# Performance work log

Hardware: AMD Instinct MI355X
Metric: run time of the kernel (lower is better)

## Reference

```python
import jax, jax.numpy as jnp
import numpy as np

B, T, D, H = 2, 4096, 512, 8
DH = D // H  # dim_head = 64


def setup_inputs() -> dict:
    key = jax.random.key(0)
    ks = jax.random.split(key, 10)
    s = 1.0 / np.sqrt(D)
    x = jax.random.normal(ks[0], (B, T, D), dtype=jnp.float32)
    Wq = jax.random.uniform(ks[1], (D, D), jnp.float32, -s, s)
    Wk = jax.random.uniform(ks[2], (D, D), jnp.float32, -s, s)
    Wv = jax.random.uniform(ks[3], (D, D), jnp.float32, -s, s)
    Wo = jax.random.uniform(ks[4], (D, D), jnp.float32, -s, s)
    bq = jnp.zeros((D,), jnp.float32)
    bk = jnp.zeros((D,), jnp.float32)
    bv = jnp.zeros((D,), jnp.float32)
    bo = jnp.zeros((D,), jnp.float32)
    mask = jax.random.randint(ks[5], (1, 1, T, T), 0, 2).astype(bool)
    return {"x": x, "Wq": Wq, "bq": bq, "Wk": Wk, "bk": bk,
            "Wv": Wv, "bv": bv, "Wo": Wo, "bo": bo, "mask": mask}


def reference(x, Wq, bq, Wk, bk, Wv, bv, Wo, bo, mask):
    # QKV projections (self-attention: Q=K=V=x)
    def split_heads(t):
        return t.reshape(B, T, H, DH).transpose(0, 2, 1, 3)  # (B,H,T,DH)
    Q = split_heads(x @ Wq + bq)
    K = split_heads(x @ Wk + bk)
    V = split_heads(x @ Wv + bv)
    # scaled dot-product attention with additive mask penalty (as in source)
    scores = jnp.einsum('bhqd,bhkd->bhqk', Q, K) / np.sqrt(DH)
    scores = scores + (~mask).astype(scores.dtype) * (-1e9)
    att_w = jax.nn.softmax(scores, axis=-1)
    O = jnp.einsum('bhqk,bhkd->bhqd', att_w, V)
    O = O.transpose(0, 2, 1, 3).reshape(B, T, D)
    return O @ Wo + bo
```

## Files before the change

kernel.cpp:

```cpp
#include <hip/hip_runtime.h>
#include <stdint.h>

#define B_ 2
#define T_ 4096
#define D_ 512
#define H_ 8
#define DH_ 64

typedef __bf16 bf16;
typedef __bf16 bf16x4_t __attribute__((ext_vector_type(4)));
typedef __bf16 bf16x8_t __attribute__((ext_vector_type(8)));
typedef float f32x4 __attribute__((ext_vector_type(4)));
typedef short short4_t __attribute__((ext_vector_type(4)));
typedef uint32_t u32;

static constexpr float QSCALE = 0.18033688011112042f;

__device__ __forceinline__ void async16(void* lds, const void* g) {
  __builtin_amdgcn_global_load_lds(
      (const __attribute__((address_space(1))) void*)g,
      (__attribute__((address_space(3))) void*)lds, 16, 0, 0);
}

__global__ __launch_bounds__(256) void prep_kernel(
    const float* __restrict__ x,
    const float* __restrict__ Wq, const float* __restrict__ Wk,
    const float* __restrict__ Wv, const float* __restrict__ Wo,
    const void* __restrict__ maskp,
    bf16* __restrict__ xb, bf16* __restrict__ WTall, bf16* __restrict__ WoT,
    u32* __restrict__ bmask)
{
  int bid = blockIdx.x;
  int tid = threadIdx.x;
  if (bid < 4096) {
    int idx = bid * 256 + tid;
    const float4* xf = (const float4*)x;
    float4 v = xf[idx];
    bf16x4_t o;
    o[0] = (bf16)v.x; o[1] = (bf16)v.y; o[2] = (bf16)v.z; o[3] = (bf16)v.w;
    ((bf16x4_t*)xb)[idx] = o;
  } else if (bid < 8192) {
    int gid = (bid - 4096) * 256 + tid;
    int sel = gid >> 18;
    int idx = gid & 262143;
    int n = idx >> 9, k = idx & 511;
    if (sel < 3) {
      const float* W = (sel == 0) ? Wq : (sel == 1) ? Wk : Wv;
      float v = W[k * 512 + n];
      if (sel == 0) v *= QSCALE;
      WTall[gid] = (bf16)v;
    } else {
      WoT[idx] = (bf16)Wo[k * 512 + n];
    }
  } else {
    int wid = (bid - 8192) * 256 + tid;
    const uint8_t* m8 = (const uint8_t*)maskp;
    bool u8mode = (__ballot(m8[4 * (tid & 63) + 1] != 0) != 0ull);
    int row = wid >> 7, wcol = wid & 127;
    size_t off = (size_t)row * 4096 + (size_t)wcol * 32;
    u32 w = 0;
    if (u8mode) {
      const uint4* p = (const uint4*)(m8 + off);
      uint4 a = p[0], b = p[1];
      u32 ws[8] = {a.x, a.y, a.z, a.w, b.x, b.y, b.z, b.w};
      #pragma unroll
      for (int j = 0; j < 32; ++j)
        if ((ws[j >> 2] >> ((j & 3) * 8)) & 0xffu) w |= (1u << j);
    } else {
      const uint4* p = (const uint4*)((const u32*)maskp + off);
      #pragma unroll
      for (int q = 0; q < 8; ++q) {
        uint4 a = p[q];
        if (a.x) w |= 1u << (q * 4 + 0);
        if (a.y) w |= 1u << (q * 4 + 1);
        if (a.z) w |= 1u << (q * 4 + 2);
        if (a.w) w |= 1u << (q * 4 + 3);
      }
    }
    bmask[((size_t)(row >> 6) * 64 + (wcol >> 1)) * 128 + (row & 63) * 2 + (wcol & 1)] = w;
  }
}

__global__ __launch_bounds__(256) void qkv_kernel(
    const bf16* __restrict__ xb, const bf16* __restrict__ WTall,
    const float* __restrict__ bq, const float* __restrict__ bk,
    const float* __restrict__ bv,
    bf16* __restrict__ Qb, bf16* __restrict__ Kb, bf16* __restrict__ Vtb)
{
  __shared__ char smem[32768];
  char* smX = smem;
  char* smW = smem + 16384;
  int tid = threadIdx.x;
  int lane = tid & 63, wave = tid >> 6;
  int lo = lane & 15, quad = lane >> 4;
  int wr = wave >> 1, wc = wave & 1;
  int bm = blockIdx.x * 128;
  int bn = blockIdx.y * 128;
  int sel = bn >> 9;
  f32x4 acc[4][4] = {};
  for (int kc = 0; kc < 8; ++kc) {
    __syncthreads();
    for (int s = tid; s < 1024; s += 256) {
      int row = s >> 3, slot = s & 7, cg = slot ^ (row & 7);
      async16(smX + s * 16, xb + (size_t)(bm + row) * 512 + kc * 64 + cg * 8);
      async16(smW + s * 16, WTall + (size_t)(bn + row) * 512 + kc * 64 + cg * 8);
    }
    __syncthreads();
    #pragma unroll
    for (int ks = 0; ks < 2; ++ks) {
      bf16x8_t a[4], b[4];
      #pragma unroll
      for (int mt = 0; mt < 4; ++mt) {
        int row = wr * 64 + mt * 16 + lo;
        int ch = (ks * 4 + quad) ^ (row & 7);
        a[mt] = *(const bf16x8_t*)(smX + row * 128 + ch * 16);
      }
      #pragma unroll
      for (int nt = 0; nt < 4; ++nt) {
        int row = wc * 64 + nt * 16 + lo;
        int ch = (ks * 4 + quad) ^ (row & 7);
        b[nt] = *(const bf16x8_t*)(smW + row * 128 + ch * 16);
      }
      if (sel < 2) {
        #pragma unroll
        for (int mt = 0; mt < 4; ++mt)
          #pragma unroll
          for (int nt = 0; nt < 4; ++nt)
            acc[mt][nt] = __builtin_amdgcn_mfma_f32_16x16x32_bf16(
                b[nt], a[mt], acc[mt][nt], 0, 0, 0);
      } else {
        #pragma unroll
        for (int mt = 0; mt < 4; ++mt)
          #pragma unroll
          for (int nt = 0; nt < 4; ++nt)
            acc[mt][nt] = __builtin_amdgcn_mfma_f32_16x16x32_bf16(
                a[mt], b[nt], acc[mt][nt], 0, 0, 0);
      }
    }
  }
  int b_ = bm >> 12;
  if (sel < 2) {
    const float* bias = (sel == 0) ? bq : bk;
    bf16* base = (sel == 0) ? Qb : Kb;
    #pragma unroll
    for (int mt = 0; mt < 4; ++mt) {
      int t = (bm & 4095) + wr * 64 + mt * 16 + lo;
      #pragma unroll
      for (int nt = 0; nt < 4; ++nt) {
        int n0 = (bn + wc * 64 + nt * 16 + quad * 4) & 511;
        int h = n0 >> 6, dh0 = n0 & 63;
        bf16x4_t v;
        #pragma unroll
        for (int r = 0; r < 4; ++r) {
          float bs = bias[n0 + r];
          if (sel == 0) bs *= QSCALE;
          v[r] = (bf16)(acc[mt][nt][r] + bs);
        }
        *(bf16x4_t*)(base + (size_t)(b_ * H_ + h) * T_ * DH_ +
                     (size_t)t * 64 + dh0) = v;
      }
    }
  } else {
    #pragma unroll
    for (int nt = 0; nt < 4; ++nt) {
      int n0 = (bn + wc * 64 + nt * 16 + lo) & 511;
      int h = n0 >> 6, dh = n0 & 63;
      float bs = bv[n0];
      #pragma unroll
      for (int mt = 0; mt < 4; ++mt) {
        int t0 = (bm & 4095) + wr * 64 + mt * 16 + quad * 4;
        bf16x4_t v;
        #pragma unroll
        for (int r = 0; r < 4; ++r) v[r] = (bf16)(acc[mt][nt][r] + bs);
        *(bf16x4_t*)(Vtb + ((size_t)(b_ * H_ + h) * DH_ + dh) * T_ + t0) = v;
      }
    }
  }
}

__global__ __launch_bounds__(256, 4) void attn_kernel(
    const bf16* __restrict__ Qb, const bf16* __restrict__ Kb,
    const bf16* __restrict__ Vtb, const u32* __restrict__ bm2,
    bf16* __restrict__ Obuf)
{
  __shared__ char smem[17408];
  char* smK = smem;
  char* smV = smem + 8192;
  u32* smM = (u32*)(smem + 16384);
  float* smLa = (float*)(smem + 16896);
  float* smLb = (float*)(smem + 17152);
  int tid = threadIdx.x;
  int lane = tid & 63, wave = tid >> 6;
  int lo = lane & 15, quad = lane >> 4;
  int qh = wave & 1, kh = wave >> 1;
  int bh = blockIdx.x >> 6;
  int qt64 = blockIdx.x & 63;
  int qbase = qt64 * 64;

  const bf16* Qg = Qb + ((size_t)bh * T_ + qbase + qh * 32) * DH_;
  bf16x8_t qf[2][2];
  #pragma unroll
  for (int qt = 0; qt < 2; ++qt)
    #pragma unroll
    for (int ks = 0; ks < 2; ++ks)
      qf[qt][ks] = *(const bf16x8_t*)(Qg + (qt * 16 + lo) * 64 + ks * 32 + quad * 8);

  short one = (lo == 0) ? (short)0x3F80 : (short)0;
  short4_t ones = {one, one, one, one};

  f32x4 O[2][4] = {};
  f32x4 Ol[2] = {};

  const bf16* Kg = Kb + (size_t)bh * T_ * DH_;
  const bf16* Vg = Vtb + (size_t)bh * DH_ * T_;
  const u32* mg = bm2 + (size_t)qt64 * 8192;

  for (int kc = 0; kc < 64; ++kc) {
    __syncthreads();
    for (int s = tid; s < 512; s += 256) {
      int row = s >> 3, slot = s & 7, cg = slot ^ (row & 7);
      async16(smK + s * 16, Kg + (size_t)(kc * 64 + row) * 64 + cg * 8);
      async16(smV + s * 16, Vg + (size_t)row * T_ + kc * 64 + cg * 8);
    }
    if (tid < 32) async16((char*)smM + tid * 16, mg + kc * 128 + tid * 4);
    __syncthreads();
    f32x4 St[2][2] = {};
    #pragma unroll
    for (int ks = 0; ks < 2; ++ks)
      #pragma unroll
      for (int kt = 0; kt < 2; ++kt) {
        int krow = kh * 32 + kt * 16 + lo;
        int ch = (ks * 4 + quad) ^ (krow & 7);
        bf16x8_t kf = *(const bf16x8_t*)(smK + krow * 128 + ch * 16);
        #pragma unroll
        for (int qt = 0; qt < 2; ++qt)
          St[kt][qt] = __builtin_amdgcn_mfma_f32_16x16x32_bf16(
              kf, qf[qt][ks], St[kt][qt], 0, 0, 0);
      }
    short4_t pf[2][2];
    #pragma unroll
    for (int qt = 0; qt < 2; ++qt) {
      u32 w = smM[(qh * 32 + qt * 16 + lo) * 2 + kh] >> (quad * 4);
      #pragma unroll
      for (int kt = 0; kt < 2; ++kt) {
        bf16x4_t t;
        #pragma unroll
        for (int r = 0; r < 4; ++r) {
          int mb = ((int)(w << (31 - (kt * 16 + r)))) >> 31;
          u32 pe = __builtin_bit_cast(u32, __builtin_amdgcn_exp2f(St[kt][qt][r]));
          t[r] = __builtin_bit_cast(bf16,
                   (unsigned short)(__builtin_bit_cast(float, pe & (u32)mb) == 0.f
                        ? 0 : 0));
          t[r] = (bf16)__builtin_bit_cast(float, pe & (u32)mb);
        }
        pf[qt][kt] = __builtin_bit_cast(short4_t, t);
      }
    }
    #pragma unroll
    for (int kt = 0; kt < 2; ++kt)
      #pragma unroll
      for (int qt = 0; qt < 2; ++qt)
        Ol[qt] = __builtin_amdgcn_mfma_f32_16x16x16bf16_1k(
            pf[qt][kt], ones, Ol[qt], 0, 0, 0);
    #pragma unroll
    for (int dt = 0; dt < 4; ++dt) {
      int d = dt * 16 + lo;
      #pragma unroll
      for (int kt = 0; kt < 2; ++kt) {
        int c0 = kh * 4 + kt * 2 + (quad >> 1);
        short4_t vf = *(const short4_t*)(
            smV + d * 128 + ((c0 ^ (d & 7)) << 4) + ((quad & 1) << 3));
        #pragma unroll
        for (int qt = 0; qt < 2; ++qt)
          O[qt][dt] = __builtin_amdgcn_mfma_f32_16x16x16bf16_1k(
              pf[qt][kt], vf, O[qt][dt], 0, 0, 0);
      }
    }
  }
  __syncthreads();
  float* smO = (float*)smem;
  if (lo == 0) {
    float* dst = (kh == 0) ? smLa : smLb;
    #pragma unroll
    for (int qt = 0; qt < 2; ++qt)
      #pragma unroll
      for (int r = 0; r < 4; ++r)
        dst[qh * 32 + qt * 16 + quad * 4 + r] = Ol[qt][r];
  }
  if (kh == 1) {
    #pragma unroll
    for (int qt = 0; qt < 2; ++qt)
      #pragma unroll
      for (int dt = 0; dt < 4; ++dt)
        #pragma unroll
        for (int r = 0; r < 4; ++r)
          smO[(qh * 32 + qt * 16 + quad * 4 + r) * 64 + dt * 16 + lo] = O[qt][dt][r];
  }
  __syncthreads();
  if (kh == 0) {
    bf16* Og = Obuf + ((size_t)bh * T_ + qbase + qh * 32) * DH_;
    #pragma unroll
    for (int qt = 0; qt < 2; ++qt) {
      #pragma unroll
      for (int r = 0; r < 4; ++r) {
        int rl = qt * 16 + quad * 4 + r;
        float inv = 1.0f / (smLa[qh * 32 + rl] + smLb[qh * 32 + rl]);
        #pragma unroll
        for (int dt = 0; dt < 4; ++dt) {
          float o = (O[qt][dt][r] + smO[(qh * 32 + rl) * 64 + dt * 16 + lo]) * inv;
          Og[(size_t)rl * 64 + dt * 16 + lo] = (bf16)o;
        }
      }
    }
  }
}

__global__ __launch_bounds__(256) void proj_kernel(
    const bf16* __restrict__ Obuf, const bf16* __restrict__ WoT,
    const float* __restrict__ bo, float* __restrict__ out)
{
  __shared__ char smem[32768];
  char* smA = smem;
  char* smW = smem + 16384;
  int tid = threadIdx.x;
  int lane = tid & 63, wave = tid >> 6;
  int lo = lane & 15, quad = lane >> 4;
  int wr = wave >> 1, wc = wave & 1;
  int bm = blockIdx.x * 128;
  int bn = blockIdx.y * 128;
  int b_ = bm >> 12, trow = bm & 4095;
  f32x4 acc[4][4] = {};
  for (int kc = 0; kc < 8; ++kc) {
    __syncthreads();
    const bf16* Ag = Obuf + ((size_t)(b_ * H_ + kc) * T_ + trow) * DH_;
    for (int s = tid; s < 1024; s += 256) {
      int row = s >> 3, slot = s & 7, cg = slot ^ (row & 7);
      async16(smA + s * 16, Ag + row * 64 + cg * 8);
      async16(smW + s * 16, WoT + (size_t)(bn + row) * 512 + kc * 64 + cg * 8);
    }
    __syncthreads();
    #pragma unroll
    for (int ks = 0; ks < 2; ++ks) {
      bf16x8_t a[4], b[4];
      #pragma unroll
      for (int mt = 0; mt < 4; ++mt) {
        int row = wr * 64 + mt * 16 + lo;
        int ch = (ks * 4 + quad) ^ (row & 7);
        a[mt] = *(const bf16x8_t*)(smA + row * 128 + ch * 16);
      }
      #pragma unroll
      for (int nt = 0; nt < 4; ++nt) {
        int row = wc * 64 + nt * 16 + lo;
        int ch = (ks * 4 + quad) ^ (row & 7);
        b[nt] = *(const bf16x8_t*)(smW + row * 128 + ch * 16);
      }
      #pragma unroll
      for (int mt = 0; mt < 4; ++mt)
        #pragma unroll
        for (int nt = 0; nt < 4; ++nt)
          acc[mt][nt] = __builtin_amdgcn_mfma_f32_16x16x32_bf16(
              b[nt], a[mt], acc[mt][nt], 0, 0, 0);
    }
  }
  #pragma unroll
  for (int mt = 0; mt < 4; ++mt) {
    int t = bm + wr * 64 + mt * 16 + lo;
    #pragma unroll
    for (int nt = 0; nt < 4; ++nt) {
      int c0 = bn + wc * 64 + nt * 16 + quad * 4;
      float4 v;
      v.x = acc[mt][nt][0] + bo[c0 + 0];
      v.y = acc[mt][nt][1] + bo[c0 + 1];
      v.z = acc[mt][nt][2] + bo[c0 + 2];
      v.w = acc[mt][nt][3] + bo[c0 + 3];
      *(float4*)(out + (size_t)t * 512 + c0) = v;
    }
  }
}

extern "C" void kernel_launch(void* const* d_in, const int* in_sizes, int n_in,
                              void* d_out, int out_size, void* d_ws, size_t ws_size,
                              hipStream_t stream) {
  const float* x  = (const float*)d_in[0];
  const float* Wq = (const float*)d_in[1];
  const float* bq = (const float*)d_in[2];
  const float* Wk = (const float*)d_in[3];
  const float* bk = (const float*)d_in[4];
  const float* Wv = (const float*)d_in[5];
  const float* bv = (const float*)d_in[6];
  const float* Wo = (const float*)d_in[7];
  const float* bo = (const float*)d_in[8];
  const void* maskp = d_in[9];
  float* out = (float*)d_out;

  char* w = (char*)d_ws;
  bf16* xb    = (bf16*)(w);
  bf16* WTall = (bf16*)(w + 8388608);
  bf16* WoT   = (bf16*)(w + 9961472);
  bf16* Qb    = (bf16*)(w + 10485760);
  bf16* Kb    = (bf16*)(w + 18874368);
  bf16* Vtb   = (bf16*)(w + 27262976);
  bf16* Obuf  = (bf16*)(w + 35651584);
  u32*  bmask = (u32*)(w + 44040192);

  prep_kernel<<<10240, 256, 0, stream>>>(x, Wq, Wk, Wv, Wo, maskp,
                                         xb, WTall, WoT, bmask);
  qkv_kernel<<<dim3(64, 12), 256, 0, stream>>>(xb, WTall, bq, bk, bv,
                                               Qb, Kb, Vtb);
  attn_kernel<<<1024, 256, 0, stream>>>(Qb, Kb, Vtb, bmask, Obuf);
  proj_kernel<<<dim3(64, 4), 256, 0, stream>>>(Obuf, WoT, bo, out);
}
```

Before: 296.0 us.

## Shrink GEMM tiles for more blocks and double attention K/V chunk per sync

The QKV and output-projection GEMMs drop from 128x128 to 64x64 tiles and launch four times as many blocks, so the 256 CUs get more parallel work. The attention kernel now loads 128 keys per iteration instead of 64 and processes them as two halves, halving the number of barriers and load rounds per block. The LDS swizzle gains an extra XOR term to reduce bank conflicts. In exchange, operand reuse per GEMM tile drops and the attention kernel uses about twice the LDS, which may limit occupancy.

```diff
diff --git a/kernel.cpp b/kernel.cpp
--- a/kernel.cpp
+++ b/kernel.cpp
@@ -87,52 +87,53 @@
     const float* __restrict__ bv,
     bf16* __restrict__ Qb, bf16* __restrict__ Kb, bf16* __restrict__ Vtb)
 {
-  __shared__ char smem[32768];
+  __shared__ char smem[16384];
   char* smX = smem;
-  char* smW = smem + 16384;
+  char* smW = smem + 8192;
   int tid = threadIdx.x;
   int lane = tid & 63, wave = tid >> 6;
   int lo = lane & 15, quad = lane >> 4;
   int wr = wave >> 1, wc = wave & 1;
-  int bm = blockIdx.x * 128;
-  int bn = blockIdx.y * 128;
+  int bm = blockIdx.x * 64;
+  int bn = blockIdx.y * 64;
   int sel = bn >> 9;
-  f32x4 acc[4][4] = {};
+  f32x4 acc[2][2] = {};
   for (int kc = 0; kc < 8; ++kc) {
     __syncthreads();
-    for (int s = tid; s < 1024; s += 256) {
-      int row = s >> 3, slot = s & 7, cg = slot ^ (row & 7);
+    for (int s = tid; s < 512; s += 256) {
+      int row = s >> 3, slot = s & 7;
+      int cg = slot ^ (row & 7) ^ ((row >> 3) & 1);
       async16(smX + s * 16, xb + (size_t)(bm + row) * 512 + kc * 64 + cg * 8);
       async16(smW + s * 16, WTall + (size_t)(bn + row) * 512 + kc * 64 + cg * 8);
     }
     __syncthreads();
     #pragma unroll
     for (int ks = 0; ks < 2; ++ks) {
-      bf16x8_t a[4], b[4];
-      #pragma unroll
-      for (int mt = 0; mt < 4; ++mt) {
-        int row = wr * 64 + mt * 16 + lo;
-        int ch = (ks * 4 + quad) ^ (row & 7);
+      bf16x8_t a[2], b[2];
+      #pragma unroll
+      for (int mt = 0; mt < 2; ++mt) {
+        int row = wr * 32 + mt * 16 + lo;
+        int ch = (ks * 4 + quad) ^ (row & 7) ^ ((row >> 3) & 1);
         a[mt] = *(const bf16x8_t*)(smX + row * 128 + ch * 16);
       }
       #pragma unroll
-      for (int nt = 0; nt < 4; ++nt) {
-        int row = wc * 64 + nt * 16 + lo;
-        int ch = (ks * 4 + quad) ^ (row & 7);
+      for (int nt = 0; nt < 2; ++nt) {
+        int row = wc * 32 + nt * 16 + lo;
+        int ch = (ks * 4 + quad) ^ (row & 7) ^ ((row >> 3) & 1);
         b[nt] = *(const bf16x8_t*)(smW + row * 128 + ch * 16);
       }
       if (sel < 2) {
         #pragma unroll
-        for (int mt = 0; mt < 4; ++mt)
+        for (int mt = 0; mt < 2; ++mt)
           #pragma unroll
-          for (int nt = 0; nt < 4; ++nt)
+          for (int nt = 0; nt < 2; ++nt)
             acc[mt][nt] = __builtin_amdgcn_mfma_f32_16x16x32_bf16(
                 b[nt], a[mt], acc[mt][nt], 0, 0, 0);
       } else {
         #pragma unroll
-        for (int mt = 0; mt < 4; ++mt)
+        for (int mt = 0; mt < 2; ++mt)
           #pragma unroll
-          for (int nt = 0; nt < 4; ++nt)
+          for (int nt = 0; nt < 2; ++nt)
             acc[mt][nt] = __builtin_amdgcn_mfma_f32_16x16x32_bf16(
                 a[mt], b[nt], acc[mt][nt], 0, 0, 0);
       }
@@ -143,11 +144,11 @@
     const float* bias = (sel == 0) ? bq : bk;
     bf16* base = (sel == 0) ? Qb : Kb;
     #pragma unroll
-    for (int mt = 0; mt < 4; ++mt) {
-      int t = (bm & 4095) + wr * 64 + mt * 16 + lo;
-      #pragma unroll
-      for (int nt = 0; nt < 4; ++nt) {
-        int n0 = (bn + wc * 64 + nt * 16 + quad * 4) & 511;
+    for (int mt = 0; mt < 2; ++mt) {
+      int t = (bm & 4095) + wr * 32 + mt * 16 + lo;
+      #pragma unroll
+      for (int nt = 0; nt < 2; ++nt) {
+        int n0 = (bn + wc * 32 + nt * 16 + quad * 4) & 511;
         int h = n0 >> 6, dh0 = n0 & 63;
         bf16x4_t v;
         #pragma unroll
@@ -162,13 +163,13 @@
     }
   } else {
     #pragma unroll
-    for (int nt = 0; nt < 4; ++nt) {
-      int n0 = (bn + wc * 64 + nt * 16 + lo) & 511;
+    for (int nt = 0; nt < 2; ++nt) {
+      int n0 = (bn + wc * 32 + nt * 16 + lo) & 511;
       int h = n0 >> 6, dh = n0 & 63;
       float bs = bv[n0];
       #pragma unroll
-      for (int mt = 0; mt < 4; ++mt) {
-        int t0 = (bm & 4095) + wr * 64 + mt * 16 + quad * 4;
+      for (int mt = 0; mt < 2; ++mt) {
+        int t0 = (bm & 4095) + wr * 32 + mt * 16 + quad * 4;
         bf16x4_t v;
         #pragma unroll
         for (int r = 0; r < 4; ++r) v[r] = (bf16)(acc[mt][nt][r] + bs);
@@ -183,12 +184,12 @@
     const bf16* __restrict__ Vtb, const u32* __restrict__ bm2,
     bf16* __restrict__ Obuf)
 {
-  __shared__ char smem[17408];
+  __shared__ char smem[34304];
   char* smK = smem;
-  char* smV = smem + 8192;
-  u32* smM = (u32*)(smem + 16384);
-  float* smLa = (float*)(smem + 16896);
-  float* smLb = (float*)(smem + 17152);
+  char* smV = smem + 16384;
+  u32* smM = (u32*)(smem + 32768);
+  float* smLa = (float*)(smem + 33792);
+  float* smLb = (float*)(smem + 34048);
   int tid = threadIdx.x;
   int lane = tid & 63, wave = tid >> 6;
   int lo = lane & 15, quad = lane >> 4;
@@ -215,65 +216,72 @@
   const bf16* Vg = Vtb + (size_t)bh * DH_ * T_;
   const u32* mg = bm2 + (size_t)qt64 * 8192;
 
-  for (int kc = 0; kc < 64; ++kc) {
-    __syncthreads();
-    for (int s = tid; s < 512; s += 256) {
-      int row = s >> 3, slot = s & 7, cg = slot ^ (row & 7);
-      async16(smK + s * 16, Kg + (size_t)(kc * 64 + row) * 64 + cg * 8);
-      async16(smV + s * 16, Vg + (size_t)row * T_ + kc * 64 + cg * 8);
-    }
-    if (tid < 32) async16((char*)smM + tid * 16, mg + kc * 128 + tid * 4);
-    __syncthreads();
-    f32x4 St[2][2] = {};
-    #pragma unroll
-    for (int ks = 0; ks < 2; ++ks)
-      #pragma unroll
-      for (int kt = 0; kt < 2; ++kt) {
-        int krow = kh * 32 + kt * 16 + lo;
-        int ch = (ks * 4 + quad) ^ (krow & 7);
-        bf16x8_t kf = *(const bf16x8_t*)(smK + krow * 128 + ch * 16);
+  for (int kc2 = 0; kc2 < 32; ++kc2) {
+    int kbase = kc2 * 128;
+    __syncthreads();
+    #pragma unroll
+    for (int i = 0; i < 4; ++i) {
+      int s = tid + i * 256;
+      int row = s >> 3, slot = s & 7;
+      int cg = slot ^ (row & 7) ^ ((row >> 3) & 1);
+      async16(smK + s * 16, Kg + (size_t)(kbase + row) * 64 + cg * 8);
+      int vrow = s >> 4, hh = (s >> 3) & 1;
+      int cgv = slot ^ (vrow & 7) ^ ((vrow >> 3) & 1);
+      async16(smV + s * 16, Vg + (size_t)vrow * T_ + kbase + hh * 64 + cgv * 8);
+    }
+    if (tid < 64) async16((char*)smM + tid * 16, mg + kc2 * 256 + tid * 4);
+    __syncthreads();
+    #pragma unroll
+    for (int h = 0; h < 2; ++h) {
+      f32x4 St[2][2] = {};
+      #pragma unroll
+      for (int ks = 0; ks < 2; ++ks)
+        #pragma unroll
+        for (int kt = 0; kt < 2; ++kt) {
+          int krow = h * 64 + kh * 32 + kt * 16 + lo;
+          int ch = (ks * 4 + quad) ^ (krow & 7) ^ ((krow >> 3) & 1);
+          bf16x8_t kf = *(const bf16x8_t*)(smK + krow * 128 + ch * 16);
+          #pragma unroll
+          for (int qt = 0; qt < 2; ++qt)
+            St[kt][qt] = __builtin_amdgcn_mfma_f32_16x16x32_bf16(
+                kf, qf[qt][ks], St[kt][qt], 0, 0, 0);
+        }
+      short4_t pf[2][2];
+      #pragma unroll
+      for (int qt = 0; qt < 2; ++qt) {
+        u32 w = smM[h * 128 + (qh * 32 + qt * 16 + lo) * 2 + kh] >> (quad * 4);
+        #pragma unroll
+        for (int kt = 0; kt < 2; ++kt) {
+          bf16x4_t t;
+          #pragma unroll
+          for (int r = 0; r < 4; ++r) {
+            int mb = ((int)(w << (31 - (kt * 16 + r)))) >> 31;
+            u32 pe = __builtin_bit_cast(u32, __builtin_amdgcn_exp2f(St[kt][qt][r]));
+            t[r] = (bf16)__builtin_bit_cast(float, pe & (u32)mb);
+          }
+          pf[qt][kt] = __builtin_bit_cast(short4_t, t);
+        }
+      }
+      #pragma unroll
+      for (int kt = 0; kt < 2; ++kt)
         #pragma unroll
         for (int qt = 0; qt < 2; ++qt)
-          St[kt][qt] = __builtin_amdgcn_mfma_f32_16x16x32_bf16(
-              kf, qf[qt][ks], St[kt][qt], 0, 0, 0);
-      }
-    short4_t pf[2][2];
-    #pragma unroll
-    for (int qt = 0; qt < 2; ++qt) {
-      u32 w = smM[(qh * 32 + qt * 16 + lo) * 2 + kh] >> (quad * 4);
-      #pragma unroll
-      for (int kt = 0; kt < 2; ++kt) {
-        bf16x4_t t;
-        #pragma unroll
-        for (int r = 0; r < 4; ++r) {
-          int mb = ((int)(w << (31 - (kt * 16 + r)))) >> 31;
-          u32 pe = __builtin_bit_cast(u32, __builtin_amdgcn_exp2f(St[kt][qt][r]));
-          t[r] = __builtin_bit_cast(bf16,
-                   (unsigned short)(__builtin_bit_cast(float, pe & (u32)mb) == 0.f
-                        ? 0 : 0));
-          t[r] = (bf16)__builtin_bit_cast(float, pe & (u32)mb);
+          Ol[qt] = __builtin_amdgcn_mfma_f32_16x16x16bf16_1k(
+              pf[qt][kt], ones, Ol[qt], 0, 0, 0);
+      #pragma unroll
+      for (int dt = 0; dt < 4; ++dt) {
+        int d = dt * 16 + lo;
+        #pragma unroll
+        for (int kt = 0; kt < 2; ++kt) {
+          int g = kh * 4 + kt * 2 + (quad >> 1);
+          int c = g ^ (d & 7) ^ ((d >> 3) & 1);
+          short4_t vf = *(const short4_t*)(
+              smV + d * 256 + h * 128 + c * 16 + ((quad & 1) << 3));
+          #pragma unroll
+          for (int qt = 0; qt < 2; ++qt)
+            O[qt][dt] = __builtin_amdgcn_mfma_f32_16x16x16bf16_1k(
+                pf[qt][kt], vf, O[qt][dt], 0, 0, 0);
         }
-        pf[qt][kt] = __builtin_bit_cast(short4_t, t);
-      }
-    }
-    #pragma unroll
-    for (int kt = 0; kt < 2; ++kt)
-      #pragma unroll
-      for (int qt = 0; qt < 2; ++qt)
-        Ol[qt] = __builtin_amdgcn_mfma_f32_16x16x16bf16_1k(
-            pf[qt][kt], ones, Ol[qt], 0, 0, 0);
-    #pragma unroll
-    for (int dt = 0; dt < 4; ++dt) {
-      int d = dt * 16 + lo;
-      #pragma unroll
-      for (int kt = 0; kt < 2; ++kt) {
-        int c0 = kh * 4 + kt * 2 + (quad >> 1);
-        short4_t vf = *(const short4_t*)(
-            smV + d * 128 + ((c0 ^ (d & 7)) << 4) + ((quad & 1) << 3));
-        #pragma unroll
-        for (int qt = 0; qt < 2; ++qt)
-          O[qt][dt] = __builtin_amdgcn_mfma_f32_16x16x16bf16_1k(
-              pf[qt][kt], vf, O[qt][dt], 0, 0, 0);
       }
     }
   }
@@ -319,55 +327,56 @@
     const bf16* __restrict__ Obuf, const bf16* __restrict__ WoT,
     const float* __restrict__ bo, float* __restrict__ out)
 {
-  __shared__ char smem[32768];
+  __shared__ char smem[16384];
   char* smA = smem;
-  char* smW = smem + 16384;
+  char* smW = smem + 8192;
   int tid = threadIdx.x;
   int lane = tid & 63, wave = tid >> 6;
   int lo = lane & 15, quad = lane >> 4;
   int wr = wave >> 1, wc = wave & 1;
-  int bm = blockIdx.x * 128;
-  int bn = blockIdx.y * 128;
+  int bm = blockIdx.x * 64;
+  int bn = blockIdx.y * 64;
   int b_ = bm >> 12, trow = bm & 4095;
-  f32x4 acc[4][4] = {};
+  f32x4 acc[2][2] = {};
   for (int kc = 0; kc < 8; ++kc) {
     __syncthreads();
     const bf16* Ag = Obuf + ((size_t)(b_ * H_ + kc) * T_ + trow) * DH_;
-    for (int s = tid; s < 1024; s += 256) {
-      int row = s >> 3, slot = s & 7, cg = slot ^ (row & 7);
+    for (int s = tid; s < 512; s += 256) {
+      int row = s >> 3, slot = s & 7;
+      int cg = slot ^ (row & 7) ^ ((row >> 3) & 1);
       async16(smA + s * 16, Ag + row * 64 + cg * 8);
       async16(smW + s * 16, WoT + (size_t)(bn + row) * 512 + kc * 64 + cg * 8);
     }
     __syncthreads();
     #pragma unroll
     for (int ks = 0; ks < 2; ++ks) {
-      bf16x8_t a[4], b[4];
-      #pragma unroll
-      for (int mt = 0; mt < 4; ++mt) {
-        int row = wr * 64 + mt * 16 + lo;
-        int ch = (ks * 4 + quad) ^ (row & 7);
+      bf16x8_t a[2], b[2];
+      #pragma unroll
+      for (int mt = 0; mt < 2; ++mt) {
+        int row = wr * 32 + mt * 16 + lo;
+        int ch = (ks * 4 + quad) ^ (row & 7) ^ ((row >> 3) & 1);
         a[mt] = *(const bf16x8_t*)(smA + row * 128 + ch * 16);
       }
       #pragma unroll
-      for (int nt = 0; nt < 4; ++nt) {
-        int row = wc * 64 + nt * 16 + lo;
-        int ch = (ks * 4 + quad) ^ (row & 7);
+      for (int nt = 0; nt < 2; ++nt) {
+        int row = wc * 32 + nt * 16 + lo;
+        int ch = (ks * 4 + quad) ^ (row & 7) ^ ((row >> 3) & 1);
         b[nt] = *(const bf16x8_t*)(smW + row * 128 + ch * 16);
       }
       #pragma unroll
-      for (int mt = 0; mt < 4; ++mt)
-        #pragma unroll
-        for (int nt = 0; nt < 4; ++nt)
+      for (int mt = 0; mt < 2; ++mt)
+        #pragma unroll
+        for (int nt = 0; nt < 2; ++nt)
           acc[mt][nt] = __builtin_amdgcn_mfma_f32_16x16x32_bf16(
               b[nt], a[mt], acc[mt][nt], 0, 0, 0);
     }
   }
   #pragma unroll
-  for (int mt = 0; mt < 4; ++mt) {
-    int t = bm + wr * 64 + mt * 16 + lo;
-    #pragma unroll
-    for (int nt = 0; nt < 4; ++nt) {
-      int c0 = bn + wc * 64 + nt * 16 + quad * 4;
+  for (int mt = 0; mt < 2; ++mt) {
+    int t = bm + wr * 32 + mt * 16 + lo;
+    #pragma unroll
+    for (int nt = 0; nt < 2; ++nt) {
+      int c0 = bn + wc * 32 + nt * 16 + quad * 4;
       float4 v;
       v.x = acc[mt][nt][0] + bo[c0 + 0];
       v.y = acc[mt][nt][1] + bo[c0 + 1];
@@ -405,8 +414,8 @@
 
   prep_kernel<<<10240, 256, 0, stream>>>(x, Wq, Wk, Wv, Wo, maskp,
                                          xb, WTall, WoT, bmask);
-  qkv_kernel<<<dim3(64, 12), 256, 0, stream>>>(xb, WTall, bq, bk, bv,
-                                               Qb, Kb, Vtb);
+  qkv_kernel<<<dim3(128, 24), 256, 0, stream>>>(xb, WTall, bq, bk, bv,
+                                                Qb, Kb, Vtb);
   attn_kernel<<<1024, 256, 0, stream>>>(Qb, Kb, Vtb, bmask, Obuf);
-  proj_kernel<<<dim3(64, 4), 256, 0, stream>>>(Obuf, WoT, bo, out);
-}
+  proj_kernel<<<dim3(128, 8), 256, 0, stream>>>(Obuf, WoT, bo, out);
+}
```

After: 348.4 us. 17.7% more time.
